# Kernel tuning notes

Measured on AMD Instinct MI355X. Metric: run time of the kernel, lower is better.

## Reference

```python
import jax, jax.numpy as jnp
import numpy as np

B = 1024
IN_SIZE = 8192
OUT_SIZE = 8192
CONNECTIVITY = 32
NNZ = OUT_SIZE * CONNECTIVITY  # 262144


def setup_inputs() -> dict:
    key = jax.random.key(0)
    kx, kv, ki = jax.random.split(key, 3)
    x = jax.random.normal(kx, (B, IN_SIZE), dtype=jnp.float32)
    # uniform init as in module: (rand-0.5)*2*sqrt(3/connectivity)
    scale = np.sqrt(3.0 / CONNECTIVITY)
    values = (jax.random.uniform(kv, (NNZ,), dtype=jnp.float32) - 0.5) * 2.0 * scale
    # indices_out = list(range(out_size)) * connectivity -> arange(nnz) % out_size
    idx_out = (jnp.arange(NNZ) % OUT_SIZE).astype(jnp.int32)
    # uniform distribution: randperm(nnz) % in_size ~ uniform over [0, in_size)
    idx_in = jax.random.randint(ki, (NNZ,), 0, IN_SIZE, dtype=jnp.int32)
    return {"x": x, "values": values, "idx_out": idx_out, "idx_in": idx_in,
            "out_size": OUT_SIZE}


def reference(x, values, idx_out, idx_in, out_size):
    # y[b, o] = sum over nnz k with idx_out[k]==o of values[k] * x[b, idx_in[k]]
    # (spmm(indices, values, out, in, x.T).T in the original)
    contrib = x[:, idx_in] * values[None, :]          # [B, nnz]
    y = jnp.zeros((x.shape[0], out_size), dtype=x.dtype)
    y = y.at[:, idx_out].add(contrib)                 # scatter-add over output rows
    return y
```

## Files before the change

kernel.cpp:

```cpp
#include <hip/hip_runtime.h>

#define IN_SIZE   8192
#define OUT_SIZE  8192
#define CONN      32
#define NNZ       (OUT_SIZE * CONN)
#define BATCH     1024
#define BT        8
#define OT        4096
#define NTHREADS  1024
#define OPT       (OT / NTHREADS)

typedef int          int4v   __attribute__((ext_vector_type(4)));
typedef float        float4v __attribute__((ext_vector_type(4)));
typedef unsigned int uint4v  __attribute__((ext_vector_type(4)));

__device__ __forceinline__ unsigned bf16rne(float f) {
  unsigned u = __builtin_bit_cast(unsigned, f);
  return (u + 0x7fffu + ((u >> 16) & 1u)) >> 16;
}

__global__ __launch_bounds__(256)
void pack_kernel(const float* __restrict__ values,
                 const int*   __restrict__ idx_in,
                 unsigned int* __restrict__ pk) {
  int k = blockIdx.x * 256 + threadIdx.x;
  if (k < NNZ) {
    unsigned u = __builtin_bit_cast(unsigned, values[k]);
    unsigned r = (u + 0xFFFu + ((u >> 13) & 1u)) >> 13;
    unsigned i = (unsigned)idx_in[k];
    unsigned s = ((i & 3u) << 11) | (i >> 2);
    pk[k] = (s << 19) | (r & 0x7FFFFu);
  }
}

template<bool PACKED>
__global__ __launch_bounds__(NTHREADS)
void spl_kernel(const float* __restrict__ x,
                const unsigned int* __restrict__ pk,
                const float* __restrict__ values,
                const int* __restrict__ idx_in,
                float* __restrict__ y) {
  __shared__ uint4v xs[IN_SIZE];

  const int bid = blockIdx.x;
  const int oh  = bid >> 7;
  const int bb  = bid & 127;
  const int b0  = bb * BT;
  const int t   = threadIdx.x;
  const int o0  = oh * OT + t * OPT;

  #pragma unroll
  for (int p = 0; p < IN_SIZE / (NTHREADS * 4); ++p) {
    int c4 = p * NTHREADS + t;
    float4v r[BT];
    #pragma unroll
    for (int b = 0; b < BT; ++b)
      r[b] = *(const float4v*)(x + (size_t)(b0 + b) * IN_SIZE + c4 * 4);
    #pragma unroll
    for (int q = 0; q < 4; ++q) {
      uint4v w;
      w.x = bf16rne(r[0][q]) | (bf16rne(r[1][q]) << 16);
      w.y = bf16rne(r[2][q]) | (bf16rne(r[3][q]) << 16);
      w.z = bf16rne(r[4][q]) | (bf16rne(r[5][q]) << 16);
      w.w = bf16rne(r[6][q]) | (bf16rne(r[7][q]) << 16);
      xs[q * 2048 + c4] = w;
    }
  }
  __syncthreads();

  float acc[OPT][BT];
  #pragma unroll
  for (int q = 0; q < OPT; ++q)
    #pragma unroll
    for (int bt = 0; bt < BT; ++bt) acc[q][bt] = 0.0f;

  const char* xsb = (const char*)xs;

  #pragma unroll 2
  for (int j = 0; j < CONN; ++j) {
    const int kb = j * OUT_SIZE + o0;
    unsigned pv[OPT];
    if constexpr (PACKED) {
      uint4v p0 = *(const uint4v*)(pk + kb);
      pv[0] = p0.x; pv[1] = p0.y; pv[2] = p0.z; pv[3] = p0.w;
    } else {
      int4v i0 = *(const int4v*)(idx_in + kb);
      float4v v0 = *(const float4v*)(values + kb);
      #pragma unroll
      for (int q = 0; q < OPT; ++q) {
        unsigned u = __builtin_bit_cast(unsigned, v0[q]);
        unsigned r = (u >> 13) & 0x7FFFFu;
        unsigned i = (unsigned)i0[q];
        pv[q] = ((((i & 3u) << 11) | (i >> 2)) << 19) | r;
      }
    }
    #pragma unroll
    for (int q = 0; q < OPT; ++q) {
      unsigned p = pv[q];
      float v = __builtin_bit_cast(float, p << 13);
      uint4v gv = *(const uint4v*)(xsb + ((p >> 15) & 0x1FFF0u));
      acc[q][0] += v * __builtin_bit_cast(float, gv.x << 16);
      acc[q][1] += v * __builtin_bit_cast(float, gv.x & 0xFFFF0000u);
      acc[q][2] += v * __builtin_bit_cast(float, gv.y << 16);
      acc[q][3] += v * __builtin_bit_cast(float, gv.y & 0xFFFF0000u);
      acc[q][4] += v * __builtin_bit_cast(float, gv.z << 16);
      acc[q][5] += v * __builtin_bit_cast(float, gv.z & 0xFFFF0000u);
      acc[q][6] += v * __builtin_bit_cast(float, gv.w << 16);
      acc[q][7] += v * __builtin_bit_cast(float, gv.w & 0xFFFF0000u);
    }
  }

  #pragma unroll
  for (int bt = 0; bt < BT; ++bt) {
    float* yr = y + (size_t)(b0 + bt) * OUT_SIZE + o0;
    float4v w = {acc[0][bt], acc[1][bt], acc[2][bt], acc[3][bt]};
    __builtin_nontemporal_store(w, (float4v*)yr);
  }
}

extern "C" void kernel_launch(void* const* d_in, const int* in_sizes, int n_in,
                              void* d_out, int out_size, void* d_ws, size_t ws_size,
                              hipStream_t stream) {
  const float* x      = (const float*)d_in[0];
  const float* values = (const float*)d_in[1];
  const int*   idx_in = (const int*)d_in[3];
  float*       y      = (float*)d_out;

  const dim3 grid((BATCH / BT) * (OUT_SIZE / OT));
  const dim3 blk(NTHREADS);

  if (ws_size >= (size_t)NNZ * sizeof(unsigned int)) {
    unsigned int* pk = (unsigned int*)d_ws;
    hipLaunchKernelGGL(pack_kernel, dim3(NNZ / 256), dim3(256), 0, stream,
                       values, idx_in, pk);
    hipLaunchKernelGGL((spl_kernel<true>), grid, blk, 0, stream,
                       x, pk, values, idx_in, y);
  } else {
    hipLaunchKernelGGL((spl_kernel<false>), grid, blk, 0, stream,
                       x, nullptr, values, idx_in, y);
  }
}
```

Baseline: 34.82 us.

## Software-pipeline packed index loads and LDS gathers, use packed float2 FMAs

Restructures the packed main loop into a software pipeline. Index words are prefetched two iterations ahead and LDS gathers one iteration ahead of the FMAs that consume them. The accumulators become float2 vectors so the compiler can emit packed FP32 multiply-adds, and launch bounds now request 4 blocks per CU. The aim is to hide global and LDS latency and cut the VALU instruction count, at the cost of extra registers for in-flight data. The pipeline prologue also issues redundant loads of row 0 on the last iterations.

```diff
diff --git a/kernel.cpp b/kernel.cpp
--- a/kernel.cpp
+++ b/kernel.cpp
@@ -11,6 +11,7 @@
 #define OPT       (OT / NTHREADS)
 
 typedef int          int4v   __attribute__((ext_vector_type(4)));
+typedef float        float2v __attribute__((ext_vector_type(2)));
 typedef float        float4v __attribute__((ext_vector_type(4)));
 typedef unsigned int uint4v  __attribute__((ext_vector_type(4)));
 
@@ -34,7 +35,7 @@
 }
 
 template<bool PACKED>
-__global__ __launch_bounds__(NTHREADS)
+__global__ __launch_bounds__(NTHREADS, 4)
 void spl_kernel(const float* __restrict__ x,
                 const unsigned int* __restrict__ pk,
                 const float* __restrict__ values,
@@ -68,53 +69,100 @@
   }
   __syncthreads();
 
-  float acc[OPT][BT];
-  #pragma unroll
-  for (int q = 0; q < OPT; ++q)
+  if constexpr (PACKED) {
+    float2v acc2[OPT][4];
     #pragma unroll
-    for (int bt = 0; bt < BT; ++bt) acc[q][bt] = 0.0f;
+    for (int q = 0; q < OPT; ++q)
+      #pragma unroll
+      for (int c = 0; c < 4; ++c) acc2[q][c] = (float2v){0.0f, 0.0f};
 
-  const char* xsb = (const char*)xs;
+    const char* xsb = (const char*)xs;
 
-  #pragma unroll 2
-  for (int j = 0; j < CONN; ++j) {
-    const int kb = j * OUT_SIZE + o0;
-    unsigned pv[OPT];
-    if constexpr (PACKED) {
-      uint4v p0 = *(const uint4v*)(pk + kb);
-      pv[0] = p0.x; pv[1] = p0.y; pv[2] = p0.z; pv[3] = p0.w;
-    } else {
+#define LDPK(J)  (*(const uint4v*)(pk + (J) * OUT_SIZE + o0))
+#define GATHER(G, P)                                                        \
+    {                                                                       \
+      _Pragma("unroll")                                                     \
+      for (int q = 0; q < OPT; ++q)                                         \
+        G[q] = *(const uint4v*)(xsb + ((P[q] >> 15) & 0x1FFF0u));           \
+    }
+#define CONSUME(P, G)                                                       \
+    {                                                                       \
+      _Pragma("unroll")                                                     \
+      for (int q = 0; q < OPT; ++q) {                                       \
+        float v = __builtin_bit_cast(float, P[q] << 13);                    \
+        float2v v2 = {v, v};                                                \
+        _Pragma("unroll")                                                   \
+        for (int c = 0; c < 4; ++c) {                                       \
+          float2v xp = {__builtin_bit_cast(float, G[q][c] << 16),           \
+                        __builtin_bit_cast(float, G[q][c] & 0xFFFF0000u)};  \
+          acc2[q][c] += v2 * xp;                                            \
+        }                                                                   \
+      }                                                                     \
+    }
+
+    uint4v pk0 = LDPK(0);
+    uint4v pk1 = LDPK(1);
+    uint4v g0[OPT];
+    GATHER(g0, pk0);
+
+    #pragma unroll
+    for (int j = 0; j < CONN; j += 2) {
+      uint4v pk2 = LDPK(j + 2 < CONN ? j + 2 : 0);
+      uint4v g1[OPT];
+      GATHER(g1, pk1);
+      CONSUME(pk0, g0);
+      uint4v pk3 = LDPK(j + 3 < CONN ? j + 3 : 0);
+      uint4v g2[OPT];
+      GATHER(g2, pk2);
+      CONSUME(pk1, g1);
+      pk0 = pk2; pk1 = pk3;
+      #pragma unroll
+      for (int q = 0; q < OPT; ++q) g0[q] = g2[q];
+    }
+#undef LDPK
+#undef GATHER
+#undef CONSUME
+
+    #pragma unroll
+    for (int bt = 0; bt < BT; ++bt) {
+      float* yr = y + (size_t)(b0 + bt) * OUT_SIZE + o0;
+      const int c = bt >> 1, h = bt & 1;
+      float4v w = {acc2[0][c][h], acc2[1][c][h], acc2[2][c][h], acc2[3][c][h]};
+      __builtin_nontemporal_store(w, (float4v*)yr);
+    }
+  } else {
+    float acc[OPT][BT];
+    #pragma unroll
+    for (int q = 0; q < OPT; ++q)
+      #pragma unroll
+      for (int bt = 0; bt < BT; ++bt) acc[q][bt] = 0.0f;
+    const char* xsb = (const char*)xs;
+    for (int j = 0; j < CONN; ++j) {
+      const int kb = j * OUT_SIZE + o0;
       int4v i0 = *(const int4v*)(idx_in + kb);
       float4v v0 = *(const float4v*)(values + kb);
       #pragma unroll
       for (int q = 0; q < OPT; ++q) {
-        unsigned u = __builtin_bit_cast(unsigned, v0[q]);
-        unsigned r = (u >> 13) & 0x7FFFFu;
         unsigned i = (unsigned)i0[q];
-        pv[q] = ((((i & 3u) << 11) | (i >> 2)) << 19) | r;
+        unsigned s = ((i & 3u) << 11) | (i >> 2);
+        float v = v0[q];
+        uint4v gv = *(const uint4v*)(xsb + (s << 4));
+        acc[q][0] += v * __builtin_bit_cast(float, gv.x << 16);
+        acc[q][1] += v * __builtin_bit_cast(float, gv.x & 0xFFFF0000u);
+        acc[q][2] += v * __builtin_bit_cast(float, gv.y << 16);
+        acc[q][3] += v * __builtin_bit_cast(float, gv.y & 0xFFFF0000u);
+        acc[q][4] += v * __builtin_bit_cast(float, gv.z << 16);
+        acc[q][5] += v * __builtin_bit_cast(float, gv.z & 0xFFFF0000u);
+        acc[q][6] += v * __builtin_bit_cast(float, gv.w << 16);
+        acc[q][7] += v * __builtin_bit_cast(float, gv.w & 0xFFFF0000u);
       }
     }
     #pragma unroll
-    for (int q = 0; q < OPT; ++q) {
-      unsigned p = pv[q];
-      float v = __builtin_bit_cast(float, p << 13);
-      uint4v gv = *(const uint4v*)(xsb + ((p >> 15) & 0x1FFF0u));
-      acc[q][0] += v * __builtin_bit_cast(float, gv.x << 16);
-      acc[q][1] += v * __builtin_bit_cast(float, gv.x & 0xFFFF0000u);
-      acc[q][2] += v * __builtin_bit_cast(float, gv.y << 16);
-      acc[q][3] += v * __builtin_bit_cast(float, gv.y & 0xFFFF0000u);
-      acc[q][4] += v * __builtin_bit_cast(float, gv.z << 16);
-      acc[q][5] += v * __builtin_bit_cast(float, gv.z & 0xFFFF0000u);
-      acc[q][6] += v * __builtin_bit_cast(float, gv.w << 16);
-      acc[q][7] += v * __builtin_bit_cast(float, gv.w & 0xFFFF0000u);
+    for (int bt = 0; bt < BT; ++bt) {
+      float* yr = y + (size_t)(b0 + bt) * OUT_SIZE + o0;
+      float4v w = {acc[0][bt], acc[1][bt], acc[2][bt], acc[3][bt]};
+      __builtin_nontemporal_store(w, (float4v*)yr);
     }
-  }
-
-  #pragma unroll
-  for (int bt = 0; bt < BT; ++bt) {
-    float* yr = y + (size_t)(b0 + bt) * OUT_SIZE + o0;
-    float4v w = {acc[0][bt], acc[1][bt], acc[2][bt], acc[3][bt]};
-    __builtin_nontemporal_store(w, (float4v*)yr);
   }
 }
 
```

After: 32.78 us. 1.06x faster.
